# Optimization experiments

Measured on AMD Instinct MI355X. Metric: run time of the kernel, lower is better.

The kernel has to match this reference:

```python
import jax, jax.numpy as jnp
import numpy as np

V_FEATS = 1024; N1 = 800; N2 = 800; K = 10
CONV = [256, 128]; DENSE = [256, 64]


def setup_inputs() -> dict:
    key = jax.random.key(0)
    ks = jax.random.split(key, 20)
    inp = {
        "Z1": jax.random.normal(ks[0], (N1, V_FEATS), jnp.float32),
        "nb1": jax.random.randint(ks[2], (N1, K), -1, N1),
        "Z2": jax.random.normal(ks[1], (N2, V_FEATS), jnp.float32),
        "nb2": jax.random.randint(ks[3], (N2, K), -1, N2),
    }
    j = 4
    dims = [V_FEATS] + CONV
    for i, (di, do) in enumerate(zip(dims[:-1], dims[1:])):
        s = 1.0 / np.sqrt(di)
        inp[f"Wr{i}"] = jax.random.normal(ks[j], (di, do), jnp.float32) * s; j += 1
        inp[f"Wnr{i}"] = jax.random.normal(ks[j], (di, do), jnp.float32) * s; j += 1
    fdims = [2 * CONV[-1]] + DENSE + [1]
    for i, (di, do) in enumerate(zip(fdims[:-1], fdims[1:])):
        s = 1.0 / np.sqrt(di)
        inp[f"fW{i}"] = jax.random.normal(ks[j], (di, do), jnp.float32) * s; j += 1
        inp[f"fb{i}"] = jnp.zeros((do,), jnp.float32)
    return inp


def gnn_layer(Z, nb, Wr, Wnr):
    # residue (self) signal and neighbor base signal
    res = Z @ Wr                                  # [N, F]
    base = Z @ Wnr                                # [N, F]
    mask = nb > -1                                # [N, K]
    feats = base[nb] * mask[..., None]            # gather (neg idx wrap, masked out)
    norm = jnp.maximum(mask.sum(1), 1).astype(Z.dtype)  # [N], avoid div-by-0
    return jax.nn.relu(res + feats.sum(1) / norm[:, None])


def _forward(Z1, nb1, Z2, nb2, Wr0, Wnr0, Wr1, Wnr1, fW0, fb0, fW1, fb1, fW2, fb2):
    # two stacked GNN layers per protein (shared weights across the two proteins)
    x1 = gnn_layer(gnn_layer(Z1, nb1, Wr0, Wnr0), nb1, Wr1, Wnr1)  # [N1, F]
    x2 = gnn_layer(gnn_layer(Z2, nb2, Wr0, Wnr0), nb2, Wr1, Wnr1)  # [N2, F]
    n1, F = x1.shape
    n2 = x2.shape[0]
    # all-pairs concat: itertools.product(rows(x1), rows(x2)) -> [N1*N2, 2F]
    pairs = jnp.concatenate(
        [jnp.broadcast_to(x1[:, None, :], (n1, n2, F)),
         jnp.broadcast_to(x2[None, :, :], (n1, n2, F))], axis=-1
    ).reshape(n1 * n2, 2 * F)
    h = jax.nn.relu(pairs @ fW0 + fb0)
    h = jax.nn.relu(h @ fW1 + fb1)
    return jnp.squeeze(h @ fW2 + fb2)             # [N1*N2]


def reference(Z1, nb1, Z2, nb2, Wr0, Wnr0, Wr1, Wnr1, fW0, fb0, fW1, fb1, fW2, fb2):
    return _forward(Z1, nb1, Z2, nb2, Wr0, Wnr0, Wr1, Wnr1,
                    fW0, fb0, fW1, fb1, fW2, fb2)
```

## Files before the change

kernel.cpp:

```cpp
#include <hip/hip_runtime.h>
#include <hip/hip_bf16.h>
#include <cstdint>
#include <cstddef>


typedef __bf16 bf16_t;
typedef __bf16 bf16x8 __attribute__((ext_vector_type(8)));
typedef float f32x4 __attribute__((ext_vector_type(4)));
typedef _Float16 f16_t;
typedef _Float16 f16x8 __attribute__((ext_vector_type(8)));

static __device__ __forceinline__ f32x4 mfma_bf16(bf16x8 a, bf16x8 b, f32x4 c) {
  return __builtin_amdgcn_mfma_f32_16x16x32_bf16(a, b, c, 0, 0, 0);
}
static __device__ __forceinline__ f32x4 mfma_f16(f16x8 a, f16x8 b, f32x4 c) {
  return __builtin_amdgcn_mfma_f32_16x16x32_f16(a, b, c, 0, 0, 0);
}

#define N1R 800
#define NR  1600
#define VF  1024
#define F0  256
#define F1  128

__global__ void conv_all(const float* __restrict__ Z1, const float* __restrict__ Z2,
                         const float* __restrict__ Wr0, const float* __restrict__ Wnr0,
                         const float* __restrict__ Wr1, const float* __restrict__ Wnr1,
                         const float* __restrict__ fW0, const float* __restrict__ fW1,
                         const float* __restrict__ fb1, const float* __restrict__ fW2,
                         const float* __restrict__ fb2,
                         bf16_t* __restrict__ Zh, bf16_t* __restrict__ Zl,
                         bf16_t* __restrict__ W0h, bf16_t* __restrict__ W0l,
                         bf16_t* __restrict__ W1h, bf16_t* __restrict__ W1l,
                         bf16_t* __restrict__ fAh, bf16_t* __restrict__ fAl,
                         bf16_t* __restrict__ fBh, bf16_t* __restrict__ fBl,
                         f16_t* __restrict__ fW1th, float* __restrict__ fbw) {
  int bx = blockIdx.x;
  if (bx < 1600) {
    int t4 = (bx * 256 + threadIdx.x) * 4;
    int r = t4 >> 10;
    int c = t4 & (VF - 1);
    float4 v = (r < N1R) ? *(const float4*)(Z1 + r * VF + c)
                         : *(const float4*)(Z2 + (r - N1R) * VF + c);
    float vv[4] = {v.x, v.y, v.z, v.w};
    #pragma unroll
    for (int u = 0; u < 4; ++u) {
      bf16_t h = (bf16_t)vv[u];
      Zh[t4 + u] = h;
      Zl[t4 + u] = (bf16_t)(vv[u] - (float)h);
    }
    return;
  }
  int wb = bx - 1600;
  if (wb >= 2560 && wb < 2624) {
    int t = (wb - 2560) * 256 + threadIdx.x;
    int n = t & 63;
    int k = t >> 6;
    fW1th[(n << 8) + k] = (f16_t)fW1[k * 64 + n];
    return;
  }
  if (wb == 2624) {
    int t = threadIdx.x;
    if (t < 128) {
      int jl = t & 15, s = t >> 4;
      fbw[jl * 8 + s] = (s < 4) ? fb1[s * 16 + jl] : fW2[(s - 4) * 16 + jl];
    } else if (t == 128) {
      fbw[128] = fb2[0];
    }
    return;
  }
  const float* src; bf16_t* dh; bf16_t* dl; int ld, lk, ln, b0;
  if      (wb < 1024) { src = Wr0;  ld = 256; lk = 10; ln = 8; dh = W0h;              dl = W0l;              b0 = 0;    }
  else if (wb < 2048) { src = Wnr0; ld = 256; lk = 10; ln = 8; dh = W0h + 256 * 1024; dl = W0l + 256 * 1024; b0 = 1024; }
  else if (wb < 2176) { src = Wr1;  ld = 128; lk = 8;  ln = 7; dh = W1h;              dl = W1l;              b0 = 2048; }
  else if (wb < 2304) { src = Wnr1; ld = 128; lk = 8;  ln = 7; dh = W1h + 128 * 256;  dl = W1l + 128 * 256;  b0 = 2176; }
  else if (wb < 2432) { src = fW0;             ld = 256; lk = 7; ln = 8; dh = fAh;    dl = fAl;              b0 = 2304; }
  else                { src = fW0 + 128 * 256; ld = 256; lk = 7; ln = 8; dh = fBh;    dl = fBl;              b0 = 2432; }
  int t = (wb - b0) * 256 + threadIdx.x;
  int n = t & ((1 << ln) - 1);
  int k = t >> ln;
  float v = src[k * ld + n];
  bf16_t h = (bf16_t)v;
  dh[(n << lk) + k] = h;
  dl[(n << lk) + k] = (bf16_t)(v - (float)h);
}

static __device__ __forceinline__ void gemm_body(
    const bf16_t* __restrict__ Ah, const bf16_t* __restrict__ Al,
    const bf16_t* __restrict__ Bth, const bf16_t* __restrict__ Btl,
    const float* __restrict__ bias, float* __restrict__ C,
    f16_t* __restrict__ Ch,
    int M, int N, int K, int kStart, int kLen, int row0b, int col0b) {
  int lane = threadIdx.x & 63;
  int w = threadIdx.x >> 6;
  int wr = w >> 1, wc = w & 1;
  int jl = lane & 15, hi = lane >> 4;

  int row0 = row0b + wr * 32;
  int col0 = col0b + wc * 32;

  int r0 = min(row0 + jl, M - 1);
  int r1 = min(row0 + 16 + jl, M - 1);
  int c0 = col0 + jl;
  int c1 = col0 + 16 + jl;

  const bf16_t* pA0h = Ah + (size_t)r0 * K + hi * 8;
  const bf16_t* pA1h = Ah + (size_t)r1 * K + hi * 8;
  const bf16_t* pA0l = Al + (size_t)r0 * K + hi * 8;
  const bf16_t* pA1l = Al + (size_t)r1 * K + hi * 8;
  const bf16_t* pB0h = Bth + (size_t)c0 * K + hi * 8;
  const bf16_t* pB1h = Bth + (size_t)c1 * K + hi * 8;
  const bf16_t* pB0l = Btl + (size_t)c0 * K + hi * 8;
  const bf16_t* pB1l = Btl + (size_t)c1 * K + hi * 8;

  f32x4 acc[2][2] = {};
  for (int kb = kStart; kb < kStart + kLen; kb += 32) {
    bf16x8 a0h = *(const bf16x8*)(pA0h + kb);
    bf16x8 a1h = *(const bf16x8*)(pA1h + kb);
    bf16x8 a0l = *(const bf16x8*)(pA0l + kb);
    bf16x8 a1l = *(const bf16x8*)(pA1l + kb);
    bf16x8 b0h = *(const bf16x8*)(pB0h + kb);
    bf16x8 b1h = *(const bf16x8*)(pB1h + kb);
    bf16x8 b0l = *(const bf16x8*)(pB0l + kb);
    bf16x8 b1l = *(const bf16x8*)(pB1l + kb);

    acc[0][0] = mfma_bf16(a0h, b0h, acc[0][0]);
    acc[0][1] = mfma_bf16(a0h, b1h, acc[0][1]);
    acc[1][0] = mfma_bf16(a1h, b0h, acc[1][0]);
    acc[1][1] = mfma_bf16(a1h, b1h, acc[1][1]);

    acc[0][0] = mfma_bf16(a0l, b0h, acc[0][0]);
    acc[0][1] = mfma_bf16(a0l, b1h, acc[0][1]);
    acc[1][0] = mfma_bf16(a1l, b0h, acc[1][0]);
    acc[1][1] = mfma_bf16(a1l, b1h, acc[1][1]);

    acc[0][0] = mfma_bf16(a0h, b0l, acc[0][0]);
    acc[0][1] = mfma_bf16(a0h, b1l, acc[0][1]);
    acc[1][0] = mfma_bf16(a1h, b0l, acc[1][0]);
    acc[1][1] = mfma_bf16(a1h, b1l, acc[1][1]);
  }

  #pragma unroll
  for (int m = 0; m < 2; ++m) {
    #pragma unroll
    for (int nn = 0; nn < 2; ++nn) {
      int col = col0 + nn * 16 + jl;
      float bv = bias ? bias[col] : 0.f;
      #pragma unroll
      for (int reg = 0; reg < 4; ++reg) {
        int row = row0 + m * 16 + hi * 4 + reg;
        if (row < M) {
          float val = acc[m][nn][reg] + bv;
          if (Ch) Ch[(size_t)row * N + col] = (f16_t)val;
          else    C[(size_t)row * N + col] = val;
        }
      }
    }
  }
}

__global__ __launch_bounds__(256) void gemm_split(
    const bf16_t* __restrict__ Ah, const bf16_t* __restrict__ Al,
    const bf16_t* __restrict__ Bth, const bf16_t* __restrict__ Btl,
    const float* __restrict__ bias, float* __restrict__ C,
    int M, int N, int K, int kLen) {
  int z = blockIdx.z;
  gemm_body(Ah, Al, Bth, Btl, bias, C + (size_t)z * M * N, nullptr,
            M, N, K, z * kLen, kLen, blockIdx.y * 64, blockIdx.x * 64);
}

__global__ __launch_bounds__(256) void gemm_dual(
    const bf16_t* __restrict__ H1h, const bf16_t* __restrict__ H1l,
    const bf16_t* __restrict__ fAh, const bf16_t* __restrict__ fAl,
    const bf16_t* __restrict__ fBh, const bf16_t* __restrict__ fBl,
    const float* __restrict__ fb0, f16_t* __restrict__ ABh) {
  int part = blockIdx.y / 13;
  int my = blockIdx.y % 13;
  gemm_body(H1h + (size_t)part * N1R * F1, H1l + (size_t)part * N1R * F1,
            part ? fBh : fAh, part ? fBl : fAl, part ? nullptr : fb0,
            nullptr, ABh + (size_t)part * N1R * 256, N1R, 256, F1, 0, F1,
            my * 64, blockIdx.x * 64);
}

__global__ void reduce_k(const float* __restrict__ P, float* __restrict__ O,
                         int count4, int S) {
  int t = blockIdx.x * blockDim.x + threadIdx.x;
  if (t >= count4) return;
  float4 s = ((const float4*)P)[t];
  for (int i = 1; i < S; ++i) {
    float4 v = *(const float4*)(P + (size_t)i * count4 * 4 + (size_t)t * 4);
    s.x += v.x; s.y += v.y; s.z += v.z; s.w += v.w;
  }
  ((float4*)O)[t] = s;
}

__global__ void agg_kernel(const float* __restrict__ RB, const int* __restrict__ nb1,
                           const int* __restrict__ nb2, bf16_t* __restrict__ Hh,
                           bf16_t* __restrict__ Hl, int F) {
  int row = blockIdx.x;
  int c = threadIdx.x;
  int S = 2 * F;
  const int* nb;
  int roff;
  if (row < N1R) { nb = nb1 + row * 10; roff = 0; }
  else           { nb = nb2 + (row - N1R) * 10; roff = N1R; }
  float s = 0.f; int cnt = 0;
  #pragma unroll
  for (int k = 0; k < 10; ++k) {
    int idx = nb[k];
    if (idx > -1) { s += RB[(size_t)(roff + idx) * S + F + c]; cnt++; }
  }
  float v = RB[(size_t)row * S + c] + s / (float)(cnt > 0 ? cnt : 1);
  v = fmaxf(v, 0.f);
  bf16_t h = (bf16_t)v;
  Hh[(size_t)row * F + c] = h;
  Hl[(size_t)row * F + c] = (bf16_t)(v - (float)h);
}

#define IBLK 2
#define ITILE 16
__global__ __launch_bounds__(256) void pair_kernel(
    const f16_t* __restrict__ ABh, const f16_t* __restrict__ W1th,
    const float* __restrict__ fbw, float* __restrict__ out) {
  __shared__ alignas(16) unsigned char sWh[64 * 512];
  __shared__ alignas(16) f16_t sA[ITILE * 256];

  const int tid = threadIdx.x;
  const int lane = tid & 63;
  const int w = tid >> 6;
  const int jl = lane & 15;
  const int hi = lane >> 4;
  const int j0 = blockIdx.x * 64;
  const int i0 = blockIdx.y * ITILE;

  #pragma unroll
  for (int s = 0; s < 8; ++s) {
    int c = tid + 256 * s;
    int n = c >> 5;
    int cb = (c & 31) << 4;
    int sw = cb ^ ((n & 7) << 4);
    *(uint4*)(sWh + n * 512 + sw) = *(const uint4*)((const unsigned char*)W1th + n * 512 + cb);
  }
  #pragma unroll
  for (int s = 0; s < 2; ++s) {
    int c = tid + 256 * s;
    int rr = c >> 5;
    int cc = c & 31;
    *(uint4*)((unsigned char*)sA + rr * 512 + cc * 16) =
        *(const uint4*)(ABh + (size_t)(i0 + rr) * 256 + cc * 8);
  }

  int j = j0 + w * 16 + jl;
  f16x8 breg[8];
  {
    const f16_t* Bp = ABh + (size_t)(N1R + j) * 256;
    bool ok = (j < N1R);
    f16x8 z{};
    #pragma unroll
    for (int t = 0; t < 8; ++t)
      breg[t] = ok ? *(const f16x8*)(Bp + t * 32 + hi * 8) : z;
  }

  float4 fb1r = *(const float4*)(fbw + jl * 8);
  float4 fw2r = *(const float4*)(fbw + jl * 8 + 4);
  float bias2 = fbw[128];

  __syncthreads();

  #pragma unroll 1
  for (int ig = 0; ig < ITILE / IBLK; ++ig) {
    f32x4 acc[IBLK][4] = {};
    #pragma unroll
    for (int t = 0; t < 8; ++t) {
      f16x8 bv = breg[t];
      f16x8 af[IBLK];
      const f16x8 Zv{};
      #pragma unroll
      for (int ib = 0; ib < IBLK; ++ib) {
        f16x8 av = *(const f16x8*)(sA + (ig * IBLK + ib) * 256 + t * 32 + hi * 8);
        af[ib] = __builtin_elementwise_max(av + bv, Zv);
      }
      int kbyte = t * 64 + hi * 16;
      #pragma unroll
      for (int nf = 0; nf < 4; ++nf) {
        int n = nf * 16 + jl;
        f16x8 wh = *(const f16x8*)(sWh + n * 512 + (kbyte ^ ((n & 7) << 4)));
        #pragma unroll
        for (int ib = 0; ib < IBLK; ++ib)
          acc[ib][nf] = mfma_f16(af[ib], wh, acc[ib][nf]);
      }
    }
    float fb1a[4] = {fb1r.x, fb1r.y, fb1r.z, fb1r.w};
    float fw2a[4] = {fw2r.x, fw2r.y, fw2r.z, fw2r.w};
    #pragma unroll
    for (int ib = 0; ib < IBLK; ++ib) {
      float part[4];
      #pragma unroll
      for (int r = 0; r < 4; ++r) {
        float ssum = 0.f;
        #pragma unroll
        for (int nf = 0; nf < 4; ++nf) {
          float h = acc[ib][nf][r] + fb1a[nf];
          h = fmaxf(h, 0.f);
          ssum += h * fw2a[nf];
        }
        part[r] = ssum;
      }
      #pragma unroll
      for (int off = 1; off < 16; off <<= 1) {
        #pragma unroll
        for (int r = 0; r < 4; ++r) part[r] += __shfl_xor(part[r], off, 64);
      }
      if (jl == 0) {
        int jo = j0 + w * 16 + hi * 4;
        if (jo < N1R) {
          float4 o = make_float4(part[0] + bias2, part[1] + bias2,
                                 part[2] + bias2, part[3] + bias2);
          *(float4*)(out + (size_t)(i0 + ig * IBLK + ib) * 800 + jo) = o;
        }
      }
    }
  }
}

extern "C" void kernel_launch(void* const* d_in, const int* in_sizes, int n_in,
                              void* d_out, int out_size, void* d_ws, size_t ws_size,
                              hipStream_t stream) {
  const float* Z1   = (const float*)d_in[0];
  const int*   nb1  = (const int*)d_in[1];
  const float* Z2   = (const float*)d_in[2];
  const int*   nb2  = (const int*)d_in[3];
  const float* Wr0  = (const float*)d_in[4];
  const float* Wnr0 = (const float*)d_in[5];
  const float* Wr1  = (const float*)d_in[6];
  const float* Wnr1 = (const float*)d_in[7];
  const float* fW0  = (const float*)d_in[8];
  const float* fb0  = (const float*)d_in[9];
  const float* fW1  = (const float*)d_in[10];
  const float* fb1  = (const float*)d_in[11];
  const float* fW2  = (const float*)d_in[12];
  const float* fb2  = (const float*)d_in[13];
  float* out = (float*)d_out;

  char* p = (char*)d_ws;
  auto alloc = [&](size_t bytes) {
    char* q = p;
    p += (bytes + 255) & ~(size_t)255;
    return q;
  };
  bf16_t* Zh    = (bf16_t*)alloc((size_t)NR * VF * 2);
  bf16_t* Zl    = (bf16_t*)alloc((size_t)NR * VF * 2);
  bf16_t* W0h   = (bf16_t*)alloc((size_t)512 * 1024 * 2);
  bf16_t* W0l   = (bf16_t*)alloc((size_t)512 * 1024 * 2);
  bf16_t* W1h   = (bf16_t*)alloc((size_t)256 * 256 * 2);
  bf16_t* W1l   = (bf16_t*)alloc((size_t)256 * 256 * 2);
  bf16_t* fAh   = (bf16_t*)alloc((size_t)256 * 128 * 2);
  bf16_t* fAl   = (bf16_t*)alloc((size_t)256 * 128 * 2);
  bf16_t* fBh   = (bf16_t*)alloc((size_t)256 * 128 * 2);
  bf16_t* fBl   = (bf16_t*)alloc((size_t)256 * 128 * 2);
  f16_t*  fW1th = (f16_t*)alloc((size_t)64 * 256 * 2);
  float*  fbw   = (float*)alloc(129 * 4);
  float*  RB0   = (float*)alloc((size_t)NR * 512 * 4);
  bf16_t* H0h   = (bf16_t*)alloc((size_t)NR * F0 * 2);
  bf16_t* H0l   = (bf16_t*)alloc((size_t)NR * F0 * 2);
  float*  RB1   = (float*)alloc((size_t)NR * 256 * 4);
  bf16_t* H1h   = (bf16_t*)alloc((size_t)NR * F1 * 2);
  bf16_t* H1l   = (bf16_t*)alloc((size_t)NR * F1 * 2);
  f16_t*  ABh   = (f16_t*)alloc((size_t)NR * 256 * 2);
  size_t part1 = (size_t)NR * 512 * 4;
  size_t part2 = (size_t)NR * 256 * 4;
  size_t used = (size_t)(p - (char*)d_ws);
  int S2 = (used + 4 * part2 + 1024 <= ws_size) ? 4 : 1;
  float* RB1p = (S2 > 1) ? (float*)alloc(4 * part2) : RB1;
  used = (size_t)(p - (char*)d_ws);
  int S = 1;
  if      (used + 8 * part1 + 1024 <= ws_size) S = 8;
  else if (used + 4 * part1 + 1024 <= ws_size) S = 4;
  else if (used + 2 * part1 + 1024 <= ws_size) S = 2;
  float* RB0p = (S > 1) ? (float*)alloc(S * part1) : RB0;
  (void)in_sizes; (void)n_in; (void)out_size;

  conv_all<<<4225, 256, 0, stream>>>(Z1, Z2, Wr0, Wnr0, Wr1, Wnr1, fW0, fW1,
                                     fb1, fW2, fb2,
                                     Zh, Zl, W0h, W0l, W1h, W1l,
                                     fAh, fAl, fBh, fBl, fW1th, fbw);
  gemm_split<<<dim3(8, 25, S), 256, 0, stream>>>(Zh, Zl, W0h, W0l, nullptr, RB0p,
                                                 NR, 512, 1024, 1024 / S);
  if (S > 1)
    reduce_k<<<(NR * 512 / 4 + 255) / 256, 256, 0, stream>>>(RB0p, RB0, NR * 512 / 4, S);
  agg_kernel<<<NR, 256, 0, stream>>>(RB0, nb1, nb2, H0h, H0l, F0);
  gemm_split<<<dim3(4, 25, S2), 256, 0, stream>>>(H0h, H0l, W1h, W1l, nullptr, RB1p,
                                                  NR, 256, 256, 256 / S2);
  if (S2 > 1)
    reduce_k<<<(NR * 256 / 4 + 255) / 256, 256, 0, stream>>>(RB1p, RB1, NR * 256 / 4, S2);
  agg_kernel<<<NR, 128, 0, stream>>>(RB1, nb1, nb2, H1h, H1l, F1);
  gemm_dual<<<dim3(4, 26), 256, 0, stream>>>(H1h, H1l, fAh, fAl, fBh, fBl, fb0, ABh);
  pair_kernel<<<dim3(13, 50), 256, 0, stream>>>(ABh, fW1th, fbw, out);
}
```

Before: 113.0 us.

## Merge pre-pair stages into one cooperative persistent kernel with grid syncs

Replaces the conversion, split-K GEMMs, reduction and aggregation kernels with a single cooperative kernel of 512 blocks that walks each stage in grid-stride loops separated by grid-wide barriers. The split-K reduction is folded into the aggregation step, which now sums the four partial buffers directly, and split-K is fixed at 4 instead of depending on workspace size. This removes several kernel launches and the separate reduce passes, but the gather now reads four partials per neighbor, and the grid syncs plus the fixed 512-block grid may limit parallelism. It also drops the workspace size check.

```diff
diff --git a/kernel.cpp b/kernel.cpp
--- a/kernel.cpp
+++ b/kernel.cpp
@@ -1,7 +1,10 @@
 #include <hip/hip_runtime.h>
 #include <hip/hip_bf16.h>
+#include <hip/hip_cooperative_groups.h>
 #include <cstdint>
 #include <cstddef>
+
+namespace cg = cooperative_groups;
 
 
 typedef __bf16 bf16_t;
@@ -23,69 +26,7 @@
 #define F0  256
 #define F1  128
 
-__global__ void conv_all(const float* __restrict__ Z1, const float* __restrict__ Z2,
-                         const float* __restrict__ Wr0, const float* __restrict__ Wnr0,
-                         const float* __restrict__ Wr1, const float* __restrict__ Wnr1,
-                         const float* __restrict__ fW0, const float* __restrict__ fW1,
-                         const float* __restrict__ fb1, const float* __restrict__ fW2,
-                         const float* __restrict__ fb2,
-                         bf16_t* __restrict__ Zh, bf16_t* __restrict__ Zl,
-                         bf16_t* __restrict__ W0h, bf16_t* __restrict__ W0l,
-                         bf16_t* __restrict__ W1h, bf16_t* __restrict__ W1l,
-                         bf16_t* __restrict__ fAh, bf16_t* __restrict__ fAl,
-                         bf16_t* __restrict__ fBh, bf16_t* __restrict__ fBl,
-                         f16_t* __restrict__ fW1th, float* __restrict__ fbw) {
-  int bx = blockIdx.x;
-  if (bx < 1600) {
-    int t4 = (bx * 256 + threadIdx.x) * 4;
-    int r = t4 >> 10;
-    int c = t4 & (VF - 1);
-    float4 v = (r < N1R) ? *(const float4*)(Z1 + r * VF + c)
-                         : *(const float4*)(Z2 + (r - N1R) * VF + c);
-    float vv[4] = {v.x, v.y, v.z, v.w};
-    #pragma unroll
-    for (int u = 0; u < 4; ++u) {
-      bf16_t h = (bf16_t)vv[u];
-      Zh[t4 + u] = h;
-      Zl[t4 + u] = (bf16_t)(vv[u] - (float)h);
-    }
-    return;
-  }
-  int wb = bx - 1600;
-  if (wb >= 2560 && wb < 2624) {
-    int t = (wb - 2560) * 256 + threadIdx.x;
-    int n = t & 63;
-    int k = t >> 6;
-    fW1th[(n << 8) + k] = (f16_t)fW1[k * 64 + n];
-    return;
-  }
-  if (wb == 2624) {
-    int t = threadIdx.x;
-    if (t < 128) {
-      int jl = t & 15, s = t >> 4;
-      fbw[jl * 8 + s] = (s < 4) ? fb1[s * 16 + jl] : fW2[(s - 4) * 16 + jl];
-    } else if (t == 128) {
-      fbw[128] = fb2[0];
-    }
-    return;
-  }
-  const float* src; bf16_t* dh; bf16_t* dl; int ld, lk, ln, b0;
-  if      (wb < 1024) { src = Wr0;  ld = 256; lk = 10; ln = 8; dh = W0h;              dl = W0l;              b0 = 0;    }
-  else if (wb < 2048) { src = Wnr0; ld = 256; lk = 10; ln = 8; dh = W0h + 256 * 1024; dl = W0l + 256 * 1024; b0 = 1024; }
-  else if (wb < 2176) { src = Wr1;  ld = 128; lk = 8;  ln = 7; dh = W1h;              dl = W1l;              b0 = 2048; }
-  else if (wb < 2304) { src = Wnr1; ld = 128; lk = 8;  ln = 7; dh = W1h + 128 * 256;  dl = W1l + 128 * 256;  b0 = 2176; }
-  else if (wb < 2432) { src = fW0;             ld = 256; lk = 7; ln = 8; dh = fAh;    dl = fAl;              b0 = 2304; }
-  else                { src = fW0 + 128 * 256; ld = 256; lk = 7; ln = 8; dh = fBh;    dl = fBl;              b0 = 2432; }
-  int t = (wb - b0) * 256 + threadIdx.x;
-  int n = t & ((1 << ln) - 1);
-  int k = t >> ln;
-  float v = src[k * ld + n];
-  bf16_t h = (bf16_t)v;
-  dh[(n << lk) + k] = h;
-  dl[(n << lk) + k] = (bf16_t)(v - (float)h);
-}
-
-static __device__ __forceinline__ void gemm_body(
+static __device__ void gemm_body(
     const bf16_t* __restrict__ Ah, const bf16_t* __restrict__ Al,
     const bf16_t* __restrict__ Bth, const bf16_t* __restrict__ Btl,
     const float* __restrict__ bias, float* __restrict__ C,
@@ -159,62 +100,150 @@
   }
 }
 
-__global__ __launch_bounds__(256) void gemm_split(
-    const bf16_t* __restrict__ Ah, const bf16_t* __restrict__ Al,
-    const bf16_t* __restrict__ Bth, const bf16_t* __restrict__ Btl,
-    const float* __restrict__ bias, float* __restrict__ C,
-    int M, int N, int K, int kLen) {
-  int z = blockIdx.z;
-  gemm_body(Ah, Al, Bth, Btl, bias, C + (size_t)z * M * N, nullptr,
-            M, N, K, z * kLen, kLen, blockIdx.y * 64, blockIdx.x * 64);
-}
-
-__global__ __launch_bounds__(256) void gemm_dual(
-    const bf16_t* __restrict__ H1h, const bf16_t* __restrict__ H1l,
-    const bf16_t* __restrict__ fAh, const bf16_t* __restrict__ fAl,
-    const bf16_t* __restrict__ fBh, const bf16_t* __restrict__ fBl,
-    const float* __restrict__ fb0, f16_t* __restrict__ ABh) {
-  int part = blockIdx.y / 13;
-  int my = blockIdx.y % 13;
-  gemm_body(H1h + (size_t)part * N1R * F1, H1l + (size_t)part * N1R * F1,
-            part ? fBh : fAh, part ? fBl : fAl, part ? nullptr : fb0,
-            nullptr, ABh + (size_t)part * N1R * 256, N1R, 256, F1, 0, F1,
-            my * 64, blockIdx.x * 64);
-}
-
-__global__ void reduce_k(const float* __restrict__ P, float* __restrict__ O,
-                         int count4, int S) {
-  int t = blockIdx.x * blockDim.x + threadIdx.x;
-  if (t >= count4) return;
-  float4 s = ((const float4*)P)[t];
-  for (int i = 1; i < S; ++i) {
-    float4 v = *(const float4*)(P + (size_t)i * count4 * 4 + (size_t)t * 4);
-    s.x += v.x; s.y += v.y; s.z += v.z; s.w += v.w;
-  }
-  ((float4*)O)[t] = s;
-}
-
-__global__ void agg_kernel(const float* __restrict__ RB, const int* __restrict__ nb1,
-                           const int* __restrict__ nb2, bf16_t* __restrict__ Hh,
-                           bf16_t* __restrict__ Hl, int F) {
-  int row = blockIdx.x;
-  int c = threadIdx.x;
-  int S = 2 * F;
-  const int* nb;
-  int roff;
-  if (row < N1R) { nb = nb1 + row * 10; roff = 0; }
-  else           { nb = nb2 + (row - N1R) * 10; roff = N1R; }
-  float s = 0.f; int cnt = 0;
-  #pragma unroll
-  for (int k = 0; k < 10; ++k) {
-    int idx = nb[k];
-    if (idx > -1) { s += RB[(size_t)(roff + idx) * S + F + c]; cnt++; }
-  }
-  float v = RB[(size_t)row * S + c] + s / (float)(cnt > 0 ? cnt : 1);
-  v = fmaxf(v, 0.f);
-  bf16_t h = (bf16_t)v;
-  Hh[(size_t)row * F + c] = h;
-  Hl[(size_t)row * F + c] = (bf16_t)(v - (float)h);
+struct P1Args {
+  const float *Z1, *Z2, *Wr0, *Wnr0, *Wr1, *Wnr1, *fW0, *fb0, *fW1, *fb1, *fW2, *fb2;
+  const int *nb1, *nb2;
+  bf16_t *Zh, *Zl, *W0h, *W0l, *W1h, *W1l, *fAh, *fAl, *fBh, *fBl;
+  f16_t *fW1th;
+  float *fbw;
+  float *RB0p, *RB1p;
+  bf16_t *H0h, *H0l, *H1h, *H1l;
+  f16_t *ABh;
+};
+
+__global__ __launch_bounds__(256, 2) void phase1_kernel(P1Args a) {
+  cg::grid_group grid = cg::this_grid();
+  const int nb = gridDim.x;
+  const int tid = threadIdx.x;
+
+  for (int bx = blockIdx.x; bx < 4225; bx += nb) {
+    if (bx < 1600) {
+      int t4 = (bx * 256 + tid) * 4;
+      int r = t4 >> 10;
+      int c = t4 & (VF - 1);
+      float4 v = (r < N1R) ? *(const float4*)(a.Z1 + r * VF + c)
+                           : *(const float4*)(a.Z2 + (r - N1R) * VF + c);
+      float vv[4] = {v.x, v.y, v.z, v.w};
+      #pragma unroll
+      for (int u = 0; u < 4; ++u) {
+        bf16_t h = (bf16_t)vv[u];
+        a.Zh[t4 + u] = h;
+        a.Zl[t4 + u] = (bf16_t)(vv[u] - (float)h);
+      }
+      continue;
+    }
+    int wb = bx - 1600;
+    if (wb >= 2560 && wb < 2624) {
+      int t = (wb - 2560) * 256 + tid;
+      int n = t & 63;
+      int k = t >> 6;
+      a.fW1th[(n << 8) + k] = (f16_t)a.fW1[k * 64 + n];
+      continue;
+    }
+    if (wb == 2624) {
+      if (tid < 128) {
+        int jl = tid & 15, s = tid >> 4;
+        a.fbw[jl * 8 + s] = (s < 4) ? a.fb1[s * 16 + jl] : a.fW2[(s - 4) * 16 + jl];
+      } else if (tid == 128) {
+        a.fbw[128] = a.fb2[0];
+      }
+      continue;
+    }
+    const float* src; bf16_t* dh; bf16_t* dl; int ld, lk, ln, b0;
+    if      (wb < 1024) { src = a.Wr0;  ld = 256; lk = 10; ln = 8; dh = a.W0h;              dl = a.W0l;              b0 = 0;    }
+    else if (wb < 2048) { src = a.Wnr0; ld = 256; lk = 10; ln = 8; dh = a.W0h + 256 * 1024; dl = a.W0l + 256 * 1024; b0 = 1024; }
+    else if (wb < 2176) { src = a.Wr1;  ld = 128; lk = 8;  ln = 7; dh = a.W1h;              dl = a.W1l;              b0 = 2048; }
+    else if (wb < 2304) { src = a.Wnr1; ld = 128; lk = 8;  ln = 7; dh = a.W1h + 128 * 256;  dl = a.W1l + 128 * 256;  b0 = 2176; }
+    else if (wb < 2432) { src = a.fW0;             ld = 256; lk = 7; ln = 8; dh = a.fAh;    dl = a.fAl;              b0 = 2304; }
+    else                { src = a.fW0 + 128 * 256; ld = 256; lk = 7; ln = 8; dh = a.fBh;    dl = a.fBl;              b0 = 2432; }
+    int t = (wb - b0) * 256 + tid;
+    int n = t & ((1 << ln) - 1);
+    int k = t >> ln;
+    float v = src[k * ld + n];
+    bf16_t h = (bf16_t)v;
+    dh[(n << lk) + k] = h;
+    dl[(n << lk) + k] = (bf16_t)(v - (float)h);
+  }
+  grid.sync();
+
+  for (int job = blockIdx.x; job < 800; job += nb) {
+    int z = job & 3, tile = job >> 2;
+    gemm_body(a.Zh, a.Zl, a.W0h, a.W0l, nullptr,
+              a.RB0p + (size_t)z * NR * 512, nullptr,
+              NR, 512, 1024, z * 256, 256, (tile >> 3) * 64, (tile & 7) * 64);
+  }
+  grid.sync();
+
+  for (int row = blockIdx.x; row < NR; row += nb) {
+    int c = tid;
+    const int* nbp; int roff;
+    if (row < N1R) { nbp = a.nb1 + row * 10; roff = 0; }
+    else           { nbp = a.nb2 + (row - N1R) * 10; roff = N1R; }
+    const size_t P = (size_t)NR * 512;
+    float s = 0.f; int cnt = 0;
+    #pragma unroll
+    for (int k = 0; k < 10; ++k) {
+      int idx = nbp[k];
+      if (idx > -1) {
+        cnt++;
+        size_t o = (size_t)(roff + idx) * 512 + 256 + c;
+        s += a.RB0p[o] + a.RB0p[o + P] + a.RB0p[o + 2 * P] + a.RB0p[o + 3 * P];
+      }
+    }
+    size_t so = (size_t)row * 512 + c;
+    float v = a.RB0p[so] + a.RB0p[so + P] + a.RB0p[so + 2 * P] + a.RB0p[so + 3 * P];
+    v += s / (float)(cnt > 0 ? cnt : 1);
+    v = fmaxf(v, 0.f);
+    bf16_t h = (bf16_t)v;
+    a.H0h[(size_t)row * F0 + c] = h;
+    a.H0l[(size_t)row * F0 + c] = (bf16_t)(v - (float)h);
+  }
+  grid.sync();
+
+  for (int job = blockIdx.x; job < 400; job += nb) {
+    int z = job & 3, tile = job >> 2;
+    gemm_body(a.H0h, a.H0l, a.W1h, a.W1l, nullptr,
+              a.RB1p + (size_t)z * NR * 256, nullptr,
+              NR, 256, 256, z * 64, 64, (tile >> 2) * 64, (tile & 3) * 64);
+  }
+  grid.sync();
+
+  for (int row = blockIdx.x; row < NR; row += nb) {
+    int c = tid;
+    if (c < F1) {
+      const int* nbp; int roff;
+      if (row < N1R) { nbp = a.nb1 + row * 10; roff = 0; }
+      else           { nbp = a.nb2 + (row - N1R) * 10; roff = N1R; }
+      const size_t P = (size_t)NR * 256;
+      float s = 0.f; int cnt = 0;
+      #pragma unroll
+      for (int k = 0; k < 10; ++k) {
+        int idx = nbp[k];
+        if (idx > -1) {
+          cnt++;
+          size_t o = (size_t)(roff + idx) * 256 + 128 + c;
+          s += a.RB1p[o] + a.RB1p[o + P] + a.RB1p[o + 2 * P] + a.RB1p[o + 3 * P];
+        }
+      }
+      size_t so = (size_t)row * 256 + c;
+      float v = a.RB1p[so] + a.RB1p[so + P] + a.RB1p[so + 2 * P] + a.RB1p[so + 3 * P];
+      v += s / (float)(cnt > 0 ? cnt : 1);
+      v = fmaxf(v, 0.f);
+      bf16_t h = (bf16_t)v;
+      a.H1h[(size_t)row * F1 + c] = h;
+      a.H1l[(size_t)row * F1 + c] = (bf16_t)(v - (float)h);
+    }
+  }
+  grid.sync();
+
+  for (int job = blockIdx.x; job < 104; job += nb) {
+    int part = (job >= 52) ? 1 : 0;
+    int rem = job - part * 52;
+    gemm_body(a.H1h + (size_t)part * N1R * F1, a.H1l + (size_t)part * N1R * F1,
+              part ? a.fBh : a.fAh, part ? a.fBl : a.fAl, part ? nullptr : a.fb0,
+              nullptr, a.ABh + (size_t)part * N1R * 256, N1R, 256, F1, 0, F1,
+              (rem >> 2) * 64, (rem & 3) * 64);
+  }
 }
 
 #define IBLK 2
@@ -326,20 +355,21 @@
 extern "C" void kernel_launch(void* const* d_in, const int* in_sizes, int n_in,
                               void* d_out, int out_size, void* d_ws, size_t ws_size,
                               hipStream_t stream) {
-  const float* Z1   = (const float*)d_in[0];
-  const int*   nb1  = (const int*)d_in[1];
-  const float* Z2   = (const float*)d_in[2];
-  const int*   nb2  = (const int*)d_in[3];
-  const float* Wr0  = (const float*)d_in[4];
-  const float* Wnr0 = (const float*)d_in[5];
-  const float* Wr1  = (const float*)d_in[6];
-  const float* Wnr1 = (const float*)d_in[7];
-  const float* fW0  = (const float*)d_in[8];
-  const float* fb0  = (const float*)d_in[9];
-  const float* fW1  = (const float*)d_in[10];
-  const float* fb1  = (const float*)d_in[11];
-  const float* fW2  = (const float*)d_in[12];
-  const float* fb2  = (const float*)d_in[13];
+  P1Args a;
+  a.Z1   = (const float*)d_in[0];
+  a.nb1  = (const int*)d_in[1];
+  a.Z2   = (const float*)d_in[2];
+  a.nb2  = (const int*)d_in[3];
+  a.Wr0  = (const float*)d_in[4];
+  a.Wnr0 = (const float*)d_in[5];
+  a.Wr1  = (const float*)d_in[6];
+  a.Wnr1 = (const float*)d_in[7];
+  a.fW0  = (const float*)d_in[8];
+  a.fb0  = (const float*)d_in[9];
+  a.fW1  = (const float*)d_in[10];
+  a.fb1  = (const float*)d_in[11];
+  a.fW2  = (const float*)d_in[12];
+  a.fb2  = (const float*)d_in[13];
   float* out = (float*)d_out;
 
   char* p = (char*)d_ws;
@@ -348,52 +378,30 @@
     p += (bytes + 255) & ~(size_t)255;
     return q;
   };
-  bf16_t* Zh    = (bf16_t*)alloc((size_t)NR * VF * 2);
-  bf16_t* Zl    = (bf16_t*)alloc((size_t)NR * VF * 2);
-  bf16_t* W0h   = (bf16_t*)alloc((size_t)512 * 1024 * 2);
-  bf16_t* W0l   = (bf16_t*)alloc((size_t)512 * 1024 * 2);
-  bf16_t* W1h   = (bf16_t*)alloc((size_t)256 * 256 * 2);
-  bf16_t* W1l   = (bf16_t*)alloc((size_t)256 * 256 * 2);
-  bf16_t* fAh   = (bf16_t*)alloc((size_t)256 * 128 * 2);
-  bf16_t* fAl   = (bf16_t*)alloc((size_t)256 * 128 * 2);
-  bf16_t* fBh   = (bf16_t*)alloc((size_t)256 * 128 * 2);
-  bf16_t* fBl   = (bf16_t*)alloc((size_t)256 * 128 * 2);
-  f16_t*  fW1th = (f16_t*)alloc((size_t)64 * 256 * 2);
-  float*  fbw   = (float*)alloc(129 * 4);
-  float*  RB0   = (float*)alloc((size_t)NR * 512 * 4);
-  bf16_t* H0h   = (bf16_t*)alloc((size_t)NR * F0 * 2);
-  bf16_t* H0l   = (bf16_t*)alloc((size_t)NR * F0 * 2);
-  float*  RB1   = (float*)alloc((size_t)NR * 256 * 4);
-  bf16_t* H1h   = (bf16_t*)alloc((size_t)NR * F1 * 2);
-  bf16_t* H1l   = (bf16_t*)alloc((size_t)NR * F1 * 2);
-  f16_t*  ABh   = (f16_t*)alloc((size_t)NR * 256 * 2);
-  size_t part1 = (size_t)NR * 512 * 4;
-  size_t part2 = (size_t)NR * 256 * 4;
-  size_t used = (size_t)(p - (char*)d_ws);
-  int S2 = (used + 4 * part2 + 1024 <= ws_size) ? 4 : 1;
-  float* RB1p = (S2 > 1) ? (float*)alloc(4 * part2) : RB1;
-  used = (size_t)(p - (char*)d_ws);
-  int S = 1;
-  if      (used + 8 * part1 + 1024 <= ws_size) S = 8;
-  else if (used + 4 * part1 + 1024 <= ws_size) S = 4;
-  else if (used + 2 * part1 + 1024 <= ws_size) S = 2;
-  float* RB0p = (S > 1) ? (float*)alloc(S * part1) : RB0;
-  (void)in_sizes; (void)n_in; (void)out_size;
-
-  conv_all<<<4225, 256, 0, stream>>>(Z1, Z2, Wr0, Wnr0, Wr1, Wnr1, fW0, fW1,
-                                     fb1, fW2, fb2,
-                                     Zh, Zl, W0h, W0l, W1h, W1l,
-                                     fAh, fAl, fBh, fBl, fW1th, fbw);
-  gemm_split<<<dim3(8, 25, S), 256, 0, stream>>>(Zh, Zl, W0h, W0l, nullptr, RB0p,
-                                                 NR, 512, 1024, 1024 / S);
-  if (S > 1)
-    reduce_k<<<(NR * 512 / 4 + 255) / 256, 256, 0, stream>>>(RB0p, RB0, NR * 512 / 4, S);
-  agg_kernel<<<NR, 256, 0, stream>>>(RB0, nb1, nb2, H0h, H0l, F0);
-  gemm_split<<<dim3(4, 25, S2), 256, 0, stream>>>(H0h, H0l, W1h, W1l, nullptr, RB1p,
-                                                  NR, 256, 256, 256 / S2);
-  if (S2 > 1)
-    reduce_k<<<(NR * 256 / 4 + 255) / 256, 256, 0, stream>>>(RB1p, RB1, NR * 256 / 4, S2);
-  agg_kernel<<<NR, 128, 0, stream>>>(RB1, nb1, nb2, H1h, H1l, F1);
-  gemm_dual<<<dim3(4, 26), 256, 0, stream>>>(H1h, H1l, fAh, fAl, fBh, fBl, fb0, ABh);
-  pair_kernel<<<dim3(13, 50), 256, 0, stream>>>(ABh, fW1th, fbw, out);
-}
+  a.Zh    = (bf16_t*)alloc((size_t)NR * VF * 2);
+  a.Zl    = (bf16_t*)alloc((size_t)NR * VF * 2);
+  a.W0h   = (bf16_t*)alloc((size_t)512 * 1024 * 2);
+  a.W0l   = (bf16_t*)alloc((size_t)512 * 1024 * 2);
+  a.W1h   = (bf16_t*)alloc((size_t)256 * 256 * 2);
+  a.W1l   = (bf16_t*)alloc((size_t)256 * 256 * 2);
+  a.fAh   = (bf16_t*)alloc((size_t)256 * 128 * 2);
+  a.fAl   = (bf16_t*)alloc((size_t)256 * 128 * 2);
+  a.fBh   = (bf16_t*)alloc((size_t)256 * 128 * 2);
+  a.fBl   = (bf16_t*)alloc((size_t)256 * 128 * 2);
+  a.fW1th = (f16_t*)alloc((size_t)64 * 256 * 2);
+  a.fbw   = (float*)alloc(129 * 4);
+  a.RB0p  = (float*)alloc((size_t)4 * NR * 512 * 4);
+  a.RB1p  = (float*)alloc((size_t)4 * NR * 256 * 4);
+  a.H0h   = (bf16_t*)alloc((size_t)NR * F0 * 2);
+  a.H0l   = (bf16_t*)alloc((size_t)NR * F0 * 2);
+  a.H1h   = (bf16_t*)alloc((size_t)NR * F1 * 2);
+  a.H1l   = (bf16_t*)alloc((size_t)NR * F1 * 2);
+  a.ABh   = (f16_t*)alloc((size_t)NR * 256 * 2);
+  (void)in_sizes; (void)n_in; (void)out_size; (void)ws_size;
+
+  P1Args ha = a;
+  void* kargs[] = { &ha };
+  hipLaunchCooperativeKernel((void*)phase1_kernel, dim3(512), dim3(256),
+                             kargs, 0, stream);
+  pair_kernel<<<dim3(13, 50), 256, 0, stream>>>(a.ABh, a.fW1th, a.fbw, out);
+}
```

Measured after the change: 445.7 us. 294% more time.

## Fuse Z bf16 split into first GEMM and fold split-K reduction into aggregation

Applied to the files above, without the earlier changes.

The first conv GEMM now reads fp32 Z directly and splits each value into bf16 hi/lo parts in registers, so the Zh/Zl staging pass in the conversion kernel goes away. The separate split-K reduce kernels are removed: the aggregation kernel sums the S partial slices itself, including for each neighbor gather. The first layer's split factor is capped at 4 instead of 8. This saves two launches and the write and re-read of the Z split buffers, but the aggregation now does S-times more gathered reads and the GEMM reads fp32 without LDS staging.

```diff
diff --git a/kernel.cpp b/kernel.cpp
--- a/kernel.cpp
+++ b/kernel.cpp
@@ -23,35 +23,17 @@
 #define F0  256
 #define F1  128
 
-__global__ void conv_all(const float* __restrict__ Z1, const float* __restrict__ Z2,
-                         const float* __restrict__ Wr0, const float* __restrict__ Wnr0,
-                         const float* __restrict__ Wr1, const float* __restrict__ Wnr1,
-                         const float* __restrict__ fW0, const float* __restrict__ fW1,
-                         const float* __restrict__ fb1, const float* __restrict__ fW2,
-                         const float* __restrict__ fb2,
-                         bf16_t* __restrict__ Zh, bf16_t* __restrict__ Zl,
-                         bf16_t* __restrict__ W0h, bf16_t* __restrict__ W0l,
-                         bf16_t* __restrict__ W1h, bf16_t* __restrict__ W1l,
-                         bf16_t* __restrict__ fAh, bf16_t* __restrict__ fAl,
-                         bf16_t* __restrict__ fBh, bf16_t* __restrict__ fBl,
-                         f16_t* __restrict__ fW1th, float* __restrict__ fbw) {
-  int bx = blockIdx.x;
-  if (bx < 1600) {
-    int t4 = (bx * 256 + threadIdx.x) * 4;
-    int r = t4 >> 10;
-    int c = t4 & (VF - 1);
-    float4 v = (r < N1R) ? *(const float4*)(Z1 + r * VF + c)
-                         : *(const float4*)(Z2 + (r - N1R) * VF + c);
-    float vv[4] = {v.x, v.y, v.z, v.w};
-    #pragma unroll
-    for (int u = 0; u < 4; ++u) {
-      bf16_t h = (bf16_t)vv[u];
-      Zh[t4 + u] = h;
-      Zl[t4 + u] = (bf16_t)(vv[u] - (float)h);
-    }
-    return;
-  }
-  int wb = bx - 1600;
+__global__ void conv_w(const float* __restrict__ Wr0, const float* __restrict__ Wnr0,
+                       const float* __restrict__ Wr1, const float* __restrict__ Wnr1,
+                       const float* __restrict__ fW0, const float* __restrict__ fW1,
+                       const float* __restrict__ fb1, const float* __restrict__ fW2,
+                       const float* __restrict__ fb2,
+                       bf16_t* __restrict__ W0h, bf16_t* __restrict__ W0l,
+                       bf16_t* __restrict__ W1h, bf16_t* __restrict__ W1l,
+                       bf16_t* __restrict__ fAh, bf16_t* __restrict__ fAl,
+                       bf16_t* __restrict__ fBh, bf16_t* __restrict__ fBl,
+                       f16_t* __restrict__ fW1th, float* __restrict__ fbw) {
+  int wb = blockIdx.x;
   if (wb >= 2560 && wb < 2624) {
     int t = (wb - 2560) * 256 + threadIdx.x;
     int n = t & 63;
@@ -85,6 +67,84 @@
   dl[(n << lk) + k] = (bf16_t)(v - (float)h);
 }
 
+static __device__ __forceinline__ void split8(float4 va, float4 vb,
+                                              bf16x8& h8, bf16x8& l8) {
+  float v[8] = {va.x, va.y, va.z, va.w, vb.x, vb.y, vb.z, vb.w};
+  #pragma unroll
+  for (int e = 0; e < 8; ++e) {
+    bf16_t h = (bf16_t)v[e];
+    h8[e] = h;
+    l8[e] = (bf16_t)(v[e] - (float)h);
+  }
+}
+
+__global__ __launch_bounds__(256) void gemm_z(
+    const float* __restrict__ Z1, const float* __restrict__ Z2,
+    const bf16_t* __restrict__ Bth, const bf16_t* __restrict__ Btl,
+    float* __restrict__ Cp, int kLen) {
+  int lane = threadIdx.x & 63;
+  int w = threadIdx.x >> 6;
+  int wr = w >> 1, wc = w & 1;
+  int jl = lane & 15, hi = lane >> 4;
+
+  int row0 = blockIdx.y * 64 + wr * 32;
+  int col0 = blockIdx.x * 64 + wc * 32;
+  int z = blockIdx.z;
+  int kStart = z * kLen;
+  float* C = Cp + (size_t)z * NR * 512;
+
+  int r0 = row0 + jl;
+  int r1 = row0 + 16 + jl;
+  int c0 = col0 + jl;
+  int c1 = col0 + 16 + jl;
+
+  const float* pZ0 = ((r0 < N1R) ? Z1 + (size_t)r0 * VF : Z2 + (size_t)(r0 - N1R) * VF) + hi * 8;
+  const float* pZ1 = ((r1 < N1R) ? Z1 + (size_t)r1 * VF : Z2 + (size_t)(r1 - N1R) * VF) + hi * 8;
+  const bf16_t* pB0h = Bth + (size_t)c0 * 1024 + hi * 8;
+  const bf16_t* pB1h = Bth + (size_t)c1 * 1024 + hi * 8;
+  const bf16_t* pB0l = Btl + (size_t)c0 * 1024 + hi * 8;
+  const bf16_t* pB1l = Btl + (size_t)c1 * 1024 + hi * 8;
+
+  f32x4 acc[2][2] = {};
+  for (int kb = kStart; kb < kStart + kLen; kb += 32) {
+    bf16x8 a0h, a0l, a1h, a1l;
+    split8(*(const float4*)(pZ0 + kb), *(const float4*)(pZ0 + kb + 4), a0h, a0l);
+    split8(*(const float4*)(pZ1 + kb), *(const float4*)(pZ1 + kb + 4), a1h, a1l);
+    bf16x8 b0h = *(const bf16x8*)(pB0h + kb);
+    bf16x8 b1h = *(const bf16x8*)(pB1h + kb);
+    bf16x8 b0l = *(const bf16x8*)(pB0l + kb);
+    bf16x8 b1l = *(const bf16x8*)(pB1l + kb);
+
+    acc[0][0] = mfma_bf16(a0h, b0h, acc[0][0]);
+    acc[0][1] = mfma_bf16(a0h, b1h, acc[0][1]);
+    acc[1][0] = mfma_bf16(a1h, b0h, acc[1][0]);
+    acc[1][1] = mfma_bf16(a1h, b1h, acc[1][1]);
+
+    acc[0][0] = mfma_bf16(a0l, b0h, acc[0][0]);
+    acc[0][1] = mfma_bf16(a0l, b1h, acc[0][1]);
+    acc[1][0] = mfma_bf16(a1l, b0h, acc[1][0]);
+    acc[1][1] = mfma_bf16(a1l, b1h, acc[1][1]);
+
+    acc[0][0] = mfma_bf16(a0h, b0l, acc[0][0]);
+    acc[0][1] = mfma_bf16(a0h, b1l, acc[0][1]);
+    acc[1][0] = mfma_bf16(a1h, b0l, acc[1][0]);
+    acc[1][1] = mfma_bf16(a1h, b1l, acc[1][1]);
+  }
+
+  #pragma unroll
+  for (int m = 0; m < 2; ++m) {
+    #pragma unroll
+    for (int nn = 0; nn < 2; ++nn) {
+      int col = col0 + nn * 16 + jl;
+      #pragma unroll
+      for (int reg = 0; reg < 4; ++reg) {
+        int row = row0 + m * 16 + hi * 4 + reg;
+        C[(size_t)row * 512 + col] = acc[m][nn][reg];
+      }
+    }
+  }
+}
+
 static __device__ __forceinline__ void gemm_body(
     const bf16_t* __restrict__ Ah, const bf16_t* __restrict__ Al,
     const bf16_t* __restrict__ Bth, const bf16_t* __restrict__ Btl,
@@ -162,10 +222,9 @@
 __global__ __launch_bounds__(256) void gemm_split(
     const bf16_t* __restrict__ Ah, const bf16_t* __restrict__ Al,
     const bf16_t* __restrict__ Bth, const bf16_t* __restrict__ Btl,
-    const float* __restrict__ bias, float* __restrict__ C,
-    int M, int N, int K, int kLen) {
+    float* __restrict__ Cp, int M, int N, int K, int kLen) {
   int z = blockIdx.z;
-  gemm_body(Ah, Al, Bth, Btl, bias, C + (size_t)z * M * N, nullptr,
+  gemm_body(Ah, Al, Bth, Btl, nullptr, Cp + (size_t)z * M * N, nullptr,
             M, N, K, z * kLen, kLen, blockIdx.y * 64, blockIdx.x * 64);
 }
 
@@ -182,24 +241,13 @@
             my * 64, blockIdx.x * 64);
 }
 
-__global__ void reduce_k(const float* __restrict__ P, float* __restrict__ O,
-                         int count4, int S) {
-  int t = blockIdx.x * blockDim.x + threadIdx.x;
-  if (t >= count4) return;
-  float4 s = ((const float4*)P)[t];
-  for (int i = 1; i < S; ++i) {
-    float4 v = *(const float4*)(P + (size_t)i * count4 * 4 + (size_t)t * 4);
-    s.x += v.x; s.y += v.y; s.z += v.z; s.w += v.w;
-  }
-  ((float4*)O)[t] = s;
-}
-
-__global__ void agg_kernel(const float* __restrict__ RB, const int* __restrict__ nb1,
+__global__ void agg_kernel(const float* __restrict__ RBp, const int* __restrict__ nb1,
                            const int* __restrict__ nb2, bf16_t* __restrict__ Hh,
-                           bf16_t* __restrict__ Hl, int F) {
+                           bf16_t* __restrict__ Hl, int F, int S) {
   int row = blockIdx.x;
   int c = threadIdx.x;
-  int S = 2 * F;
+  int Sw = 2 * F;
+  const size_t P = (size_t)NR * Sw;
   const int* nb;
   int roff;
   if (row < N1R) { nb = nb1 + row * 10; roff = 0; }
@@ -208,9 +256,18 @@
   #pragma unroll
   for (int k = 0; k < 10; ++k) {
     int idx = nb[k];
-    if (idx > -1) { s += RB[(size_t)(roff + idx) * S + F + c]; cnt++; }
-  }
-  float v = RB[(size_t)row * S + c] + s / (float)(cnt > 0 ? cnt : 1);
+    if (idx > -1) {
+      cnt++;
+      size_t o = (size_t)(roff + idx) * Sw + F + c;
+      float t = 0.f;
+      for (int z = 0; z < S; ++z) t += RBp[o + (size_t)z * P];
+      s += t;
+    }
+  }
+  size_t so = (size_t)row * Sw + c;
+  float v = 0.f;
+  for (int z = 0; z < S; ++z) v += RBp[so + (size_t)z * P];
+  v += s / (float)(cnt > 0 ? cnt : 1);
   v = fmaxf(v, 0.f);
   bf16_t h = (bf16_t)v;
   Hh[(size_t)row * F + c] = h;
@@ -348,8 +405,6 @@
     p += (bytes + 255) & ~(size_t)255;
     return q;
   };
-  bf16_t* Zh    = (bf16_t*)alloc((size_t)NR * VF * 2);
-  bf16_t* Zl    = (bf16_t*)alloc((size_t)NR * VF * 2);
   bf16_t* W0h   = (bf16_t*)alloc((size_t)512 * 1024 * 2);
   bf16_t* W0l   = (bf16_t*)alloc((size_t)512 * 1024 * 2);
   bf16_t* W1h   = (bf16_t*)alloc((size_t)256 * 256 * 2);
@@ -360,40 +415,29 @@
   bf16_t* fBl   = (bf16_t*)alloc((size_t)256 * 128 * 2);
   f16_t*  fW1th = (f16_t*)alloc((size_t)64 * 256 * 2);
   float*  fbw   = (float*)alloc(129 * 4);
-  float*  RB0   = (float*)alloc((size_t)NR * 512 * 4);
   bf16_t* H0h   = (bf16_t*)alloc((size_t)NR * F0 * 2);
   bf16_t* H0l   = (bf16_t*)alloc((size_t)NR * F0 * 2);
-  float*  RB1   = (float*)alloc((size_t)NR * 256 * 4);
   bf16_t* H1h   = (bf16_t*)alloc((size_t)NR * F1 * 2);
   bf16_t* H1l   = (bf16_t*)alloc((size_t)NR * F1 * 2);
   f16_t*  ABh   = (f16_t*)alloc((size_t)NR * 256 * 2);
   size_t part1 = (size_t)NR * 512 * 4;
   size_t part2 = (size_t)NR * 256 * 4;
   size_t used = (size_t)(p - (char*)d_ws);
-  int S2 = (used + 4 * part2 + 1024 <= ws_size) ? 4 : 1;
-  float* RB1p = (S2 > 1) ? (float*)alloc(4 * part2) : RB1;
-  used = (size_t)(p - (char*)d_ws);
-  int S = 1;
-  if      (used + 8 * part1 + 1024 <= ws_size) S = 8;
-  else if (used + 4 * part1 + 1024 <= ws_size) S = 4;
-  else if (used + 2 * part1 + 1024 <= ws_size) S = 2;
-  float* RB0p = (S > 1) ? (float*)alloc(S * part1) : RB0;
+  int S = 1, S2 = 1;
+  if (used + 4 * part1 + 4 * part2 + 2048 <= ws_size) { S = 4; S2 = 4; }
+  else if (used + 2 * part1 + 2 * part2 + 2048 <= ws_size) { S = 2; S2 = 2; }
+  float* RB0p = (float*)alloc(S * part1);
+  float* RB1p = (float*)alloc(S2 * part2);
   (void)in_sizes; (void)n_in; (void)out_size;
 
-  conv_all<<<4225, 256, 0, stream>>>(Z1, Z2, Wr0, Wnr0, Wr1, Wnr1, fW0, fW1,
-                                     fb1, fW2, fb2,
-                                     Zh, Zl, W0h, W0l, W1h, W1l,
-                                     fAh, fAl, fBh, fBl, fW1th, fbw);
-  gemm_split<<<dim3(8, 25, S), 256, 0, stream>>>(Zh, Zl, W0h, W0l, nullptr, RB0p,
-                                                 NR, 512, 1024, 1024 / S);
-  if (S > 1)
-    reduce_k<<<(NR * 512 / 4 + 255) / 256, 256, 0, stream>>>(RB0p, RB0, NR * 512 / 4, S);
-  agg_kernel<<<NR, 256, 0, stream>>>(RB0, nb1, nb2, H0h, H0l, F0);
-  gemm_split<<<dim3(4, 25, S2), 256, 0, stream>>>(H0h, H0l, W1h, W1l, nullptr, RB1p,
+  conv_w<<<2625, 256, 0, stream>>>(Wr0, Wnr0, Wr1, Wnr1, fW0, fW1, fb1, fW2, fb2,
+                                   W0h, W0l, W1h, W1l, fAh, fAl, fBh, fBl,
+                                   fW1th, fbw);
+  gemm_z<<<dim3(8, 25, S), 256, 0, stream>>>(Z1, Z2, W0h, W0l, RB0p, 1024 / S);
+  agg_kernel<<<NR, 256, 0, stream>>>(RB0p, nb1, nb2, H0h, H0l, F0, S);
+  gemm_split<<<dim3(4, 25, S2), 256, 0, stream>>>(H0h, H0l, W1h, W1l, RB1p,
                                                   NR, 256, 256, 256 / S2);
-  if (S2 > 1)
-    reduce_k<<<(NR * 256 / 4 + 255) / 256, 256, 0, stream>>>(RB1p, RB1, NR * 256 / 4, S2);
-  agg_kernel<<<NR, 128, 0, stream>>>(RB1, nb1, nb2, H1h, H1l, F1);
+  agg_kernel<<<NR, 128, 0, stream>>>(RB1p, nb1, nb2, H1h, H1l, F1, S2);
   gemm_dual<<<dim3(4, 26), 256, 0, stream>>>(H1h, H1l, fAh, fAl, fBh, fBl, fb0, ABh);
   pair_kernel<<<dim3(13, 50), 256, 0, stream>>>(ABh, fW1th, fbw, out);
 }
```

Measured after the change: 119.5 us. 5.8% more time.
